# Kernel optimization log

Hardware: AMD Instinct MI355X
Metric: run time of the kernel (lower is better)

Reference implementation:

```python
import jax, jax.numpy as jnp
import numpy as np
import math

L, D, H, HD, F, G, V, P = 15, 512, 64, 8, 2048, 128, 7, 49
B, N = 4, 256


def setup_inputs() -> dict:
    key = jax.random.key(0)
    ks = jax.random.split(key, 24)
    nrm = lambda k, shape, s=0.02: (jax.random.normal(k, shape) * s).astype(jnp.float32)
    inp = {}
    inp["atom_types"] = jax.random.randint(ks[0], (B, N), 0, V)
    inp["coords"] = jax.random.normal(ks[1], (B, N, 3)) * 3.0
    inp["pair_types"] = jax.random.randint(ks[2], (B, N, N), 0, P)
    inp["mask"] = jnp.ones((B, N), dtype=bool)
    # embeddings / pair encoding params
    inp["atom_emb"] = nrm(ks[3], (V, D), 1.0).at[0].set(0.0)  # padding_idx=0
    inp["gaussian_mu"] = jax.random.normal(ks[4], (G,))
    inp["gaussian_sigma"] = jnp.ones((G,)) * 0.1
    inp["pair_a"] = jax.random.normal(ks[5], (P,)) * 0.01
    inp["pair_b"] = jax.random.normal(ks[6], (P,)) * 0.01
    inp["pl_w"] = nrm(ks[7], (G,))
    inp["pl_b"] = jnp.zeros(())
    # stacked per-layer params (leading dim L for lax.scan)
    inp["ln1_g"] = jnp.ones((L, D)); inp["ln1_b"] = jnp.zeros((L, D))
    inp["qkv_w"] = nrm(ks[8], (L, 3 * D, D)); inp["qkv_b"] = jnp.zeros((L, 3 * D))
    inp["pp_w"] = nrm(ks[9], (L, H), 0.1); inp["pp_b"] = jnp.zeros((L, H))
    inp["out_w"] = nrm(ks[10], (L, D, D)); inp["out_b"] = jnp.zeros((L, D))
    inp["ln2_g"] = jnp.ones((L, D)); inp["ln2_b"] = jnp.zeros((L, D))
    inp["ffn_w1"] = nrm(ks[11], (L, F, D)); inp["ffn_b1"] = jnp.zeros((L, F))
    inp["ffn_w2"] = nrm(ks[12], (L, D, F)); inp["ffn_b2"] = jnp.zeros((L, D))
    # SE3 head scalar affines (Linear(1,1) twice) and energy head
    inp["se3_uw"] = jnp.array(0.5); inp["se3_ub"] = jnp.array(0.01)
    inp["se3_ww"] = jnp.array(0.5); inp["se3_wb"] = jnp.array(0.01)
    inp["en_w"] = nrm(ks[13], (D,)); inp["en_b"] = jnp.zeros(())
    return inp


def _layernorm(x, g, b):
    m = x.mean(-1, keepdims=True)
    v = ((x - m) ** 2).mean(-1, keepdims=True)
    return (x - m) / jnp.sqrt(v + 1e-5) * g + b


def reference(atom_types, coords, pair_types, mask,
              atom_emb, gaussian_mu, gaussian_sigma, pair_a, pair_b, pl_w, pl_b,
              ln1_g, ln1_b, qkv_w, qkv_b, pp_w, pp_b, out_w, out_b,
              ln2_g, ln2_b, ffn_w1, ffn_b1, ffn_w2, ffn_b2,
              se3_uw, se3_ub, se3_ww, se3_wb, en_w, en_b):
    b_, n_ = atom_types.shape
    h = atom_emb[atom_types]  # [B,N,D]

    delta = coords[:, :, None, :] - coords[:, None, :, :]  # [B,N,N,3]
    d2 = (delta ** 2).sum(-1)
    dist = jnp.sqrt(jnp.maximum(d2, 1e-12))  # safe norm (grad-safe at 0)
    dist = jnp.where(mask[:, :, None], dist, 0.0)
    da = (pair_a[pair_types] * dist + pair_b[pair_types])[..., None]  # [B,N,N,1]
    gt = jnp.exp(-(da - gaussian_mu) ** 2) / (2.0 * gaussian_sigma ** 2)
    gt = gt / (gaussian_sigma * math.sqrt(2.0 * math.pi))
    gt = gt * mask[:, :, None, None]  # [B,N,N,G]
    pair_repr = gt @ pl_w + pl_b  # [B,N,N]
    pair_mask = mask[:, :, None] & mask[:, None, :]
    pair_repr = pair_repr * pair_mask

    scale = 1.0 / math.sqrt(HD)
    row_mask = mask[:, None, :, None]  # masks query rows, per original code

    def layer(hc, p):
        (l1g, l1b, qw, qb, ppw, ppb, ow, ob, l2g, l2b, w1, b1, w2, b2) = p
        x = _layernorm(hc, l1g, l1b)
        qkv = (x @ qw.T + qb).reshape(b_, n_, 3, H, HD)
        q, k, v = qkv[:, :, 0], qkv[:, :, 1], qkv[:, :, 2]
        scores = jnp.einsum('bnhd,bmhd->bhnm', q, k) * scale
        bias = pair_repr[..., None] * ppw + ppb  # [B,N,N,H]
        scores = scores + bias.transpose(0, 3, 1, 2)
        scores = jnp.where(row_mask, scores, -1e9)
        probs = jax.nn.softmax(scores, axis=-1)
        probs = jnp.where(jnp.isnan(probs), 0.0, probs)
        attn = jnp.einsum('bhnm,bmhd->bnhd', probs, v).reshape(b_, n_, D)
        hc = hc + attn @ ow.T + ob
        x2 = _layernorm(hc, l2g, l2b)
        ffn = jax.nn.gelu(x2 @ w1.T + b1, approximate=False) @ w2.T + b2
        return hc + ffn, None

    h, _ = jax.lax.scan(layer, h, (ln1_g, ln1_b, qkv_w, qkv_b, pp_w, pp_b,
                                   out_w, out_b, ln2_g, ln2_b,
                                   ffn_w1, ffn_b1, ffn_w2, ffn_b2))

    # --- SE3 equivariant head ---
    c = jax.nn.relu(pair_repr)[..., None]  # [B,N,N,1]
    c = c * se3_uw + se3_ub
    c = c * se3_ww + se3_wb
    c = c * mask[:, :, None, None]
    update = (delta * c).sum(axis=2)  # [B,N,3]
    num_valid = mask.sum(-1).astype(coords.dtype)[:, None, None] + 1e-6
    pred_coords = coords + update / num_valid

    cls = h[:, 0, :]
    pred_energy = cls @ en_w + en_b  # [B]
    return pred_coords, pred_energy


if __name__ == '__main__':
    out = reference(**setup_inputs())
    print(out[0].shape, out[1].shape)
```

## Files before the change

### kernel.cpp

```cpp
#include <hip/hip_runtime.h>
#include <hip/hip_bf16.h>
#include <math.h>

#define LAY 15
#define DIM 512
#define NH 64
#define HD 8
#define FF 2048
#define NG 128
#define BATCH 4
#define NTOK 256
#define PSTRIDE 524288

typedef __attribute__((ext_vector_type(8))) short short8;
typedef __attribute__((ext_vector_type(4))) short short4v;
typedef __attribute__((ext_vector_type(2))) short short2v;
typedef __attribute__((ext_vector_type(8))) __bf16 bf16x8;
typedef __attribute__((ext_vector_type(4))) float f32x4;

__device__ inline short f2bs(float f) {
  __bf16 b = (__bf16)f;
  return __builtin_bit_cast(short, b);
}

__global__ __launch_bounds__(256) void embed_kernel(
    const int* __restrict__ types, const float* __restrict__ emb,
    float* __restrict__ h)
{
  int idx = blockIdx.x * 256 + threadIdx.x;
  int token = idx >> 9;
  int d = idx & 511;
  h[idx] = emb[types[token] * DIM + d];
}

__global__ __launch_bounds__(256) void cvt_kernel(
    const float* __restrict__ qkvw, const float* __restrict__ outw,
    const float* __restrict__ w1, const float* __restrict__ w2,
    short* __restrict__ dst)
{
  const int G = 2949120;
  int t0 = blockIdx.x * 256 + threadIdx.x;
  f32x4 f[4];
#pragma unroll
  for (int r = 0; r < 4; ++r) {
    int i = t0 + r * G;
    const float* src; int off;
    if (i < 2949120)      { src = qkvw; off = i; }
    else if (i < 3932160) { src = outw; off = i - 2949120; }
    else if (i < 7864320) { src = w1;   off = i - 3932160; }
    else                  { src = w2;   off = i - 7864320; }
    f[r] = __builtin_nontemporal_load((const f32x4*)src + off);
  }
#pragma unroll
  for (int r = 0; r < 4; ++r) {
    int i = t0 + r * G;
    short4v o;
    o[0] = f2bs(f[r][0]); o[1] = f2bs(f[r][1]);
    o[2] = f2bs(f[r][2]); o[3] = f2bs(f[r][3]);
    *(short4v*)(dst + (size_t)i * 4) = o;
  }
}

__global__ __launch_bounds__(256) void pair_kernel(
    const int* __restrict__ pair_types, const float* __restrict__ coords,
    const float* __restrict__ mu, const float* __restrict__ sigma,
    const float* __restrict__ pa, const float* __restrict__ pb,
    const float* __restrict__ plw, const float* __restrict__ plb,
    const float* __restrict__ uw, const float* __restrict__ ub,
    const float* __restrict__ ww, const float* __restrict__ wb,
    float* __restrict__ pair_repr, float* __restrict__ out)
{
  __shared__ float smu[NG], sw[NG];
  __shared__ float sm[4][3];
  int tid = threadIdx.x;
  if (tid < NG) {
    float sg = sigma[tid];
    smu[tid] = mu[tid];
    sw[tid] = plw[tid] / (2.0f * sg * sg * sg * 2.5066282746310002f);
  }
  __syncthreads();
  int bi = blockIdx.x;
  int b = bi >> 8;
  int j = tid;
  int idx = bi * 256 + j;
  const float* ci = coords + bi * 3;
  const float* cj = coords + (b * NTOK + j) * 3;
  float dx = ci[0] - cj[0], dy = ci[1] - cj[1], dz = ci[2] - cj[2];
  float d2 = dx * dx + dy * dy + dz * dz;
  float dist = sqrtf(fmaxf(d2, 1e-12f));
  int pt = pair_types[idx];
  float da = pa[pt] * dist + pb[pt];
  float acc = 0.0f;
#pragma unroll 8
  for (int g = 0; g < NG; ++g) {
    float t = da - smu[g];
    acc += __expf(-t * t) * sw[g];
  }
  float pr = acc + plb[0];
  pair_repr[idx] = pr;

  float c = fmaxf(pr, 0.0f);
  c = c * uw[0] + ub[0];
  c = c * ww[0] + wb[0];
  float sx = dx * c, sy = dy * c, sz = dz * c;
#pragma unroll
  for (int o = 32; o > 0; o >>= 1) {
    sx += __shfl_xor(sx, o);
    sy += __shfl_xor(sy, o);
    sz += __shfl_xor(sz, o);
  }
  if ((j & 63) == 0) {
    sm[j >> 6][0] = sx; sm[j >> 6][1] = sy; sm[j >> 6][2] = sz;
  }
  __syncthreads();
  if (j < 3) {
    float u = sm[0][j] + sm[1][j] + sm[2][j] + sm[3][j];
    out[bi * 3 + j] = coords[bi * 3 + j] + u * (1.0f / (256.0f + 1e-6f));
  }
}

__global__ __launch_bounds__(256) void pairT_kernel(
    const float* __restrict__ pr, float* __restrict__ prT)
{
  __shared__ float tile[32][33];
  int b = blockIdx.z;
  int i0 = blockIdx.y * 32, j0 = blockIdx.x * 32;
  int tx = threadIdx.x & 31, ty = threadIdx.x >> 5;
#pragma unroll
  for (int r = 0; r < 4; ++r)
    tile[ty + r * 8][tx] = pr[((size_t)(b * NTOK + i0 + ty + r * 8)) * NTOK + j0 + tx];
  __syncthreads();
#pragma unroll
  for (int r = 0; r < 4; ++r)
    prT[((size_t)(b * NTOK + j0 + ty + r * 8)) * NTOK + i0 + tx] = tile[tx][ty + r * 8];
}

__global__ __launch_bounds__(256) void ln_kernel(
    const float* __restrict__ h, const float* __restrict__ g,
    const float* __restrict__ beta, short* __restrict__ x)
{
  int t = blockIdx.x;
  int tid = threadIdx.x;
  float2 v = *(const float2*)&h[(size_t)t * DIM + tid * 2];
  __shared__ float sm[4];
  float s = v.x + v.y;
#pragma unroll
  for (int o = 32; o > 0; o >>= 1) s += __shfl_xor(s, o);
  if ((tid & 63) == 0) sm[tid >> 6] = s;
  __syncthreads();
  float mean = (sm[0] + sm[1] + sm[2] + sm[3]) * (1.0f / 512.0f);
  float d0 = v.x - mean, d1 = v.y - mean;
  float ss = d0 * d0 + d1 * d1;
#pragma unroll
  for (int o = 32; o > 0; o >>= 1) ss += __shfl_xor(ss, o);
  __syncthreads();
  if ((tid & 63) == 0) sm[tid >> 6] = ss;
  __syncthreads();
  float var = (sm[0] + sm[1] + sm[2] + sm[3]) * (1.0f / 512.0f);
  float rstd = rsqrtf(var + 1e-5f);
  float2 gg = *(const float2*)&g[tid * 2];
  float2 bb = *(const float2*)&beta[tid * 2];
  short2v o2;
  o2[0] = f2bs(d0 * rstd * gg.x + bb.x);
  o2[1] = f2bs(d1 * rstd * gg.y + bb.y);
  *(short2v*)&x[(size_t)t * DIM + tid * 2] = o2;
}

__global__ __launch_bounds__(256) void ln_res_kernel(
    float* __restrict__ h, const float* __restrict__ part, int kparts,
    const float* __restrict__ g, const float* __restrict__ beta,
    short* __restrict__ x)
{
  int t = blockIdx.x;
  int tid = threadIdx.x;
  size_t base = (size_t)t * DIM + tid * 2;
  float2 v = *(const float2*)&h[base];
  for (int z = 0; z < kparts; ++z) {
    float2 pz = *(const float2*)&part[(size_t)z * PSTRIDE + base];
    v.x += pz.x; v.y += pz.y;
  }
  *(float2*)&h[base] = v;
  __shared__ float sm[4];
  float s = v.x + v.y;
#pragma unroll
  for (int o = 32; o > 0; o >>= 1) s += __shfl_xor(s, o);
  if ((tid & 63) == 0) sm[tid >> 6] = s;
  __syncthreads();
  float mean = (sm[0] + sm[1] + sm[2] + sm[3]) * (1.0f / 512.0f);
  float d0 = v.x - mean, d1 = v.y - mean;
  float ss = d0 * d0 + d1 * d1;
#pragma unroll
  for (int o = 32; o > 0; o >>= 1) ss += __shfl_xor(ss, o);
  __syncthreads();
  if ((tid & 63) == 0) sm[tid >> 6] = ss;
  __syncthreads();
  float var = (sm[0] + sm[1] + sm[2] + sm[3]) * (1.0f / 512.0f);
  float rstd = rsqrtf(var + 1e-5f);
  float2 gg = *(const float2*)&g[tid * 2];
  float2 bb = *(const float2*)&beta[tid * 2];
  short2v o2;
  o2[0] = f2bs(d0 * rstd * gg.x + bb.x);
  o2[1] = f2bs(d1 * rstd * gg.y + bb.y);
  *(short2v*)&x[base] = o2;
}

template <int MODE, int TSTEPS>
__global__ __launch_bounds__(64) void mm3(
    const short* __restrict__ A, const short* __restrict__ W,
    const float* __restrict__ bias, float* __restrict__ Cf,
    short* __restrict__ Cb, int N, int K)
{
  __shared__ alignas(16) short As[3][2048];
  __shared__ alignas(16) short Bs[3][4096];
  int tid = threadIdx.x;
  int fr = tid & 15, fq = (tid >> 4) & 3;
  int m0 = blockIdx.y * 32, n0 = blockIdx.x * 64;
  int kbeg = blockIdx.z * (TSTEPS * 64);

  auto stage = [&](int p, int k0) {
#pragma unroll
    for (int r = 0; r < 4; ++r) {
      int id = r * 64 + tid;
      int row = id >> 3;
      int col = (id & 7) ^ (row & 7);
      const short* ga = &A[(size_t)(m0 + row) * K + k0 + col * 8];
      __builtin_amdgcn_global_load_lds(
          (const __attribute__((address_space(1))) void*)ga,
          (__attribute__((address_space(3))) void*)&As[p][r * 512],
          16, 0, 0);
    }
#pragma unroll
    for (int r = 0; r < 8; ++r) {
      int id = r * 64 + tid;
      int row = id >> 3;
      int col = (id & 7) ^ (row & 7);
      const short* gw = &W[(size_t)(n0 + row) * K + k0 + col * 8];
      __builtin_amdgcn_global_load_lds(
          (const __attribute__((address_space(1))) void*)gw,
          (__attribute__((address_space(3))) void*)&Bs[p][r * 512],
          16, 0, 0);
    }
  };

  f32x4 acc[2][4];
#pragma unroll
  for (int i = 0; i < 2; ++i)
#pragma unroll
    for (int j = 0; j < 4; ++j) acc[i][j] = (f32x4){0.f, 0.f, 0.f, 0.f};

  int aslot[2][2], bslot[2][4];
#pragma unroll
  for (int s = 0; s < 2; ++s) {
    int c = s * 4 + fq;
#pragma unroll
    for (int i = 0; i < 2; ++i) {
      int m = i * 16 + fr;
      aslot[s][i] = m * 8 + (c ^ (m & 7));
    }
#pragma unroll
    for (int j = 0; j < 4; ++j) {
      int n = j * 16 + fr;
      bslot[s][j] = n * 8 + (c ^ (n & 7));
    }
  }

  stage(0, kbeg);
  stage(1, kbeg + 64);
  stage(2, kbeg + 128);

#pragma unroll
  for (int t = 0; t < TSTEPS; ++t) {
    if (t < TSTEPS - 2)       asm volatile("s_waitcnt vmcnt(24)" ::: "memory");
    else if (t == TSTEPS - 2) asm volatile("s_waitcnt vmcnt(12)" ::: "memory");
    else                      asm volatile("s_waitcnt vmcnt(0)" ::: "memory");
    int p = t % 3;
    short8 af[2][2], bf_[2][4];
#pragma unroll
    for (int s = 0; s < 2; ++s) {
#pragma unroll
      for (int i = 0; i < 2; ++i)
        af[s][i] = *(const short8*)&As[p][aslot[s][i] * 8];
#pragma unroll
      for (int j = 0; j < 4; ++j)
        bf_[s][j] = *(const short8*)&Bs[p][bslot[s][j] * 8];
    }
    asm volatile("s_waitcnt lgkmcnt(0)" ::: "memory");
    __builtin_amdgcn_sched_barrier(0);
    if (t + 3 < TSTEPS) stage(p, kbeg + (t + 3) * 64);
#pragma unroll
    for (int s = 0; s < 2; ++s)
#pragma unroll
      for (int i = 0; i < 2; ++i)
#pragma unroll
        for (int j = 0; j < 4; ++j)
          acc[i][j] = __builtin_amdgcn_mfma_f32_16x16x32_bf16(
              af[s][i], bf_[s][j], acc[i][j], 0, 0, 0);
  }

#pragma unroll
  for (int i = 0; i < 2; ++i) {
#pragma unroll
    for (int j = 0; j < 4; ++j) {
      int col = n0 + j * 16 + fr;
      float bcol = bias[col];
#pragma unroll
      for (int rr = 0; rr < 4; ++rr) {
        int row = m0 + i * 16 + fq * 4 + rr;
        size_t idx = (size_t)row * N + col;
        float v = acc[i][j][rr];
        if (MODE == 2) {
          v += bcol;
          Cb[idx] = f2bs(0.5f * v * (1.0f + erff(v * 0.70710678118654752f)));
        } else if (MODE == 3) {
          Cb[idx] = f2bs(v + bcol);
        } else {
          if (blockIdx.z == 0) v += bcol;
          Cf[(size_t)blockIdx.z * PSTRIDE + idx] = v;
        }
      }
    }
  }
}

__global__ __launch_bounds__(128) void attn_mfma(
    const short* __restrict__ qkv, const float* __restrict__ prT,
    const float* __restrict__ ppw, const float* __restrict__ ppb,
    short* __restrict__ attn)
{
  __shared__ alignas(16) short Kl[256 * 8];
  __shared__ alignas(16) short Ql[128 * 8];
  __shared__ alignas(16) short VT[8 * 264];
  __shared__ alignas(16) short P[2 * 16 * 264];
  __shared__ alignas(16) float linv[32];
  int h = blockIdx.x, b = blockIdx.y;
  int qbase = blockIdx.z * 128;
  int tid = threadIdx.x;

#pragma unroll
  for (int r0 = 0; r0 < 2; ++r0) {
    int r = tid + r0 * 128;
    short8 kv = *(const short8*)&qkv[(size_t)(b * NTOK + r) * 1536 + 512 + h * 8];
    *(short8*)&Kl[r * 8] = kv;
    short8 vv = *(const short8*)&qkv[(size_t)(b * NTOK + r) * 1536 + 1024 + h * 8];
#pragma unroll
    for (int d = 0; d < 8; ++d) VT[d * 264 + r] = vv[d];
  }
  {
    short8 qv = *(const short8*)&qkv[(size_t)(b * NTOK + qbase + tid) * 1536 + h * 8];
    *(short8*)&Ql[tid * 8] = qv;
  }
  __syncthreads();

  int lane = tid & 63, w = tid >> 6;
  int fr = lane & 15, quad = lane >> 4;
  float pw = ppw[h], pbb = ppb[h];
  const float scale = 0.35355339059327373f;
  short8 zero8 = {0, 0, 0, 0, 0, 0, 0, 0};

  short8 vfrag[8];
#pragma unroll
  for (int kc = 0; kc < 8; ++kc)
    vfrag[kc] = (fr < 8) ? *(const short8*)&VT[fr * 264 + kc * 32 + quad * 8]
                         : zero8;

  short* Pw = &P[w * 16 * 264];
  float* lw = &linv[w * 16];

  for (int qt = 0; qt < 4; ++qt) {
    int qloc = w * 64 + qt * 16;
    int qg = qbase + qloc + fr;
    const float* prp = &prT[(size_t)b * 65536 + qg];
    float prv[16][4];
#pragma unroll
    for (int t = 0; t < 16; ++t)
#pragma unroll
      for (int r = 0; r < 4; ++r)
        prv[t][r] = prp[(size_t)(t * 16 + quad * 4 + r) * NTOK];

    short8 qf = zero8;
    if (quad == 0) qf = *(const short8*)&Ql[(qloc + fr) * 8];
    f32x4 sacc[16];
#pragma unroll
    for (int t = 0; t < 16; ++t) {
      short8 kf = zero8;
      if (quad == 0) kf = *(const short8*)&Kl[(t * 16 + fr) * 8];
      sacc[t] = __builtin_amdgcn_mfma_f32_16x16x32_bf16(
          kf, qf, (f32x4){0.f, 0.f, 0.f, 0.f}, 0, 0, 0);
    }

    float l = 0.f;
#pragma unroll
    for (int t = 0; t < 16; ++t) {
      short4v pk;
#pragma unroll
      for (int r = 0; r < 4; ++r) {
        float s = sacc[t][r] * scale + prv[t][r] * pw + pbb;
        float p = __expf(s);
        l += p;
        pk[r] = f2bs(p);
      }
      *(short4v*)&Pw[fr * 264 + t * 16 + quad * 4] = pk;
    }
    l += __shfl_xor(l, 16);
    l += __shfl_xor(l, 32);
    if (lane < 16) lw[fr] = 1.0f / l;

    f32x4 oacc = (f32x4){0.f, 0.f, 0.f, 0.f};
#pragma unroll
    for (int kc = 0; kc < 8; ++kc) {
      short8 pf = *(const short8*)&Pw[fr * 264 + kc * 32 + quad * 8];
      oacc = __builtin_amdgcn_mfma_f32_16x16x32_bf16(pf, vfrag[kc], oacc, 0, 0, 0);
    }
    if (fr < 8) {
      f32x4 li = *(f32x4*)&lw[quad * 4];
#pragma unroll
      for (int r = 0; r < 4; ++r) {
        int q = qbase + qloc + quad * 4 + r;
        attn[(size_t)(b * NTOK + q) * DIM + h * 8 + fr] = f2bs(oacc[r] * li[r]);
      }
    }
  }
}

__global__ __launch_bounds__(256) void energy_kernel(
    const float* __restrict__ h, const float* __restrict__ part,
    const float* __restrict__ enw, const float* __restrict__ enb,
    float* __restrict__ out)
{
  int b = blockIdx.x;
  int tid = threadIdx.x;
  size_t base = (size_t)(b * NTOK) * DIM;
  float x0 = h[base + tid], x1 = h[base + tid + 256];
#pragma unroll
  for (int z = 0; z < 2; ++z) {
    x0 += part[(size_t)z * PSTRIDE + base + tid];
    x1 += part[(size_t)z * PSTRIDE + base + tid + 256];
  }
  float s = x0 * enw[tid] + x1 * enw[tid + 256];
  __shared__ float sm[4];
#pragma unroll
  for (int o = 32; o > 0; o >>= 1) s += __shfl_xor(s, o);
  if ((tid & 63) == 0) sm[tid >> 6] = s;
  __syncthreads();
  if (tid == 0) out[BATCH * NTOK * 3 + b] = sm[0] + sm[1] + sm[2] + sm[3] + enb[0];
}

extern "C" void kernel_launch(void* const* d_in, const int* in_sizes, int n_in,
                              void* d_out, int out_size, void* d_ws, size_t ws_size,
                              hipStream_t stream)
{
  const int*   atom_types = (const int*)d_in[0];
  const float* coords     = (const float*)d_in[1];
  const int*   pair_types = (const int*)d_in[2];
  const float* atom_emb = (const float*)d_in[4];
  const float* gmu  = (const float*)d_in[5];
  const float* gsig = (const float*)d_in[6];
  const float* pa   = (const float*)d_in[7];
  const float* pb   = (const float*)d_in[8];
  const float* plw  = (const float*)d_in[9];
  const float* plb  = (const float*)d_in[10];
  const float* ln1g = (const float*)d_in[11];
  const float* ln1b = (const float*)d_in[12];
  const float* qkvw = (const float*)d_in[13];
  const float* qkvb = (const float*)d_in[14];
  const float* ppw  = (const float*)d_in[15];
  const float* ppb  = (const float*)d_in[16];
  const float* outw = (const float*)d_in[17];
  const float* outb = (const float*)d_in[18];
  const float* ln2g = (const float*)d_in[19];
  const float* ln2b = (const float*)d_in[20];
  const float* w1   = (const float*)d_in[21];
  const float* b1   = (const float*)d_in[22];
  const float* w2   = (const float*)d_in[23];
  const float* b2   = (const float*)d_in[24];
  const float* uw   = (const float*)d_in[25];
  const float* ub   = (const float*)d_in[26];
  const float* sww  = (const float*)d_in[27];
  const float* swb  = (const float*)d_in[28];
  const float* enw  = (const float*)d_in[29];
  const float* enb  = (const float*)d_in[30];

  float* out = (float*)d_out;
  float* ws  = (float*)d_ws;
  float* pair_repr = ws;
  float* prT  = pair_repr + 262144;
  float* h    = prT + 262144;
  float* part = h + 524288;
  short* qkv_bf  = (short*)(part + 4 * 524288);
  short* x_bf    = qkv_bf + 1572864;
  short* attn_bf = x_bf + 524288;
  short* ffn1_bf = attn_bf + 524288;
  short* qkvw_bf = ffn1_bf + 2097152;
  short* outw_bf = qkvw_bf + 11796480;
  short* w1_bf   = outw_bf + 3932160;
  short* w2_bf   = w1_bf + 15728640;

  cvt_kernel<<<11520, 256, 0, stream>>>(qkvw, outw, w1, w2, qkvw_bf);

  embed_kernel<<<2048, 256, 0, stream>>>(atom_types, atom_emb, h);
  pair_kernel<<<1024, 256, 0, stream>>>(pair_types, coords, gmu, gsig, pa, pb,
                                        plw, plb, uw, ub, sww, swb,
                                        pair_repr, out);
  pairT_kernel<<<dim3(8, 8, 4), 256, 0, stream>>>(pair_repr, prT);

  for (int l = 0; l < LAY; ++l) {
    if (l == 0)
      ln_kernel<<<1024, 256, 0, stream>>>(h, ln1g, ln1b, x_bf);
    else
      ln_res_kernel<<<1024, 256, 0, stream>>>(h, part, 2,
                                              ln1g + l * DIM, ln1b + l * DIM, x_bf);
    mm3<3, 8><<<dim3(24, 32, 1), 64, 0, stream>>>(
        x_bf, qkvw_bf + (size_t)l * 1536 * DIM, qkvb + l * 1536, nullptr, qkv_bf,
        1536, DIM);
    attn_mfma<<<dim3(NH, BATCH, 2), 128, 0, stream>>>(
        qkv_bf, prT, ppw + l * NH, ppb + l * NH, attn_bf);
    mm3<4, 4><<<dim3(8, 32, 2), 64, 0, stream>>>(
        attn_bf, outw_bf + (size_t)l * DIM * DIM, outb + l * DIM, part, nullptr,
        DIM, DIM);
    ln_res_kernel<<<1024, 256, 0, stream>>>(h, part, 2,
                                            ln2g + l * DIM, ln2b + l * DIM, x_bf);
    mm3<2, 8><<<dim3(32, 32, 1), 64, 0, stream>>>(
        x_bf, w1_bf + (size_t)l * FF * DIM, b1 + l * FF, nullptr, ffn1_bf,
        FF, DIM);
    mm3<4, 16><<<dim3(8, 32, 2), 64, 0, stream>>>(
        ffn1_bf, w2_bf + (size_t)l * DIM * FF, b2 + l * DIM, part, nullptr,
        DIM, FF);
  }
  energy_kernel<<<BATCH, 256, 0, stream>>>(h, part, enw, enb, out);
}
```

Before: 1.113 ms.

## Load GEMM fragments directly from global into registers, dropping LDS staging

The mm3 GEMM kernel no longer stages A and W tiles through a triple-buffered LDS ring with global_load_lds. Each lane now loads its MFMA operand fragments straight from global memory into registers, double-buffered across k-steps. This removes LDS traffic, the explicit waitcnt choreography and the LDS footprint, which could raise occupancy. In exchange, global loads are less coalesced (16-byte strided row reads) and the compiler's own waits replace the manual pipelining.

```diff
diff --git a/kernel.cpp b/kernel.cpp
--- a/kernel.cpp
+++ b/kernel.cpp
@@ -210,83 +210,32 @@
     const float* __restrict__ bias, float* __restrict__ Cf,
     short* __restrict__ Cb, int N, int K)
 {
-  __shared__ alignas(16) short As[3][2048];
-  __shared__ alignas(16) short Bs[3][4096];
-  int tid = threadIdx.x;
-  int fr = tid & 15, fq = (tid >> 4) & 3;
+  int tid = threadIdx.x;
+  int fr = tid & 15, fq = tid >> 4;
   int m0 = blockIdx.y * 32, n0 = blockIdx.x * 64;
   int kbeg = blockIdx.z * (TSTEPS * 64);
 
-  auto stage = [&](int p, int k0) {
-#pragma unroll
-    for (int r = 0; r < 4; ++r) {
-      int id = r * 64 + tid;
-      int row = id >> 3;
-      int col = (id & 7) ^ (row & 7);
-      const short* ga = &A[(size_t)(m0 + row) * K + k0 + col * 8];
-      __builtin_amdgcn_global_load_lds(
-          (const __attribute__((address_space(1))) void*)ga,
-          (__attribute__((address_space(3))) void*)&As[p][r * 512],
-          16, 0, 0);
-    }
-#pragma unroll
-    for (int r = 0; r < 8; ++r) {
-      int id = r * 64 + tid;
-      int row = id >> 3;
-      int col = (id & 7) ^ (row & 7);
-      const short* gw = &W[(size_t)(n0 + row) * K + k0 + col * 8];
-      __builtin_amdgcn_global_load_lds(
-          (const __attribute__((address_space(1))) void*)gw,
-          (__attribute__((address_space(3))) void*)&Bs[p][r * 512],
-          16, 0, 0);
+  const short* Ab = A + (size_t)(m0 + fr) * K + fq * 8 + kbeg;
+  const short* Wb = W + (size_t)(n0 + fr) * K + fq * 8 + kbeg;
+
+  f32x4 acc[2][4];
+#pragma unroll
+  for (int i = 0; i < 2; ++i)
+#pragma unroll
+    for (int j = 0; j < 4; ++j) acc[i][j] = (f32x4){0.f, 0.f, 0.f, 0.f};
+
+  auto LD = [&](short8 (&af)[2][2], short8 (&bf)[2][4], int k0) {
+#pragma unroll
+    for (int s = 0; s < 2; ++s) {
+#pragma unroll
+      for (int i = 0; i < 2; ++i)
+        af[s][i] = *(const short8*)(Ab + (size_t)i * 16 * K + k0 + s * 32);
+#pragma unroll
+      for (int j = 0; j < 4; ++j)
+        bf[s][j] = *(const short8*)(Wb + (size_t)j * 16 * K + k0 + s * 32);
     }
   };
-
-  f32x4 acc[2][4];
-#pragma unroll
-  for (int i = 0; i < 2; ++i)
-#pragma unroll
-    for (int j = 0; j < 4; ++j) acc[i][j] = (f32x4){0.f, 0.f, 0.f, 0.f};
-
-  int aslot[2][2], bslot[2][4];
-#pragma unroll
-  for (int s = 0; s < 2; ++s) {
-    int c = s * 4 + fq;
-#pragma unroll
-    for (int i = 0; i < 2; ++i) {
-      int m = i * 16 + fr;
-      aslot[s][i] = m * 8 + (c ^ (m & 7));
-    }
-#pragma unroll
-    for (int j = 0; j < 4; ++j) {
-      int n = j * 16 + fr;
-      bslot[s][j] = n * 8 + (c ^ (n & 7));
-    }
-  }
-
-  stage(0, kbeg);
-  stage(1, kbeg + 64);
-  stage(2, kbeg + 128);
-
-#pragma unroll
-  for (int t = 0; t < TSTEPS; ++t) {
-    if (t < TSTEPS - 2)       asm volatile("s_waitcnt vmcnt(24)" ::: "memory");
-    else if (t == TSTEPS - 2) asm volatile("s_waitcnt vmcnt(12)" ::: "memory");
-    else                      asm volatile("s_waitcnt vmcnt(0)" ::: "memory");
-    int p = t % 3;
-    short8 af[2][2], bf_[2][4];
-#pragma unroll
-    for (int s = 0; s < 2; ++s) {
-#pragma unroll
-      for (int i = 0; i < 2; ++i)
-        af[s][i] = *(const short8*)&As[p][aslot[s][i] * 8];
-#pragma unroll
-      for (int j = 0; j < 4; ++j)
-        bf_[s][j] = *(const short8*)&Bs[p][bslot[s][j] * 8];
-    }
-    asm volatile("s_waitcnt lgkmcnt(0)" ::: "memory");
-    __builtin_amdgcn_sched_barrier(0);
-    if (t + 3 < TSTEPS) stage(p, kbeg + (t + 3) * 64);
+  auto FM = [&](short8 (&af)[2][2], short8 (&bf)[2][4]) {
 #pragma unroll
     for (int s = 0; s < 2; ++s)
 #pragma unroll
@@ -294,7 +243,20 @@
 #pragma unroll
         for (int j = 0; j < 4; ++j)
           acc[i][j] = __builtin_amdgcn_mfma_f32_16x16x32_bf16(
-              af[s][i], bf_[s][j], acc[i][j], 0, 0, 0);
+              af[s][i], bf[s][j], acc[i][j], 0, 0, 0);
+  };
+
+  short8 aA[2][2], bA[2][4], aB[2][2], bB[2][4];
+  LD(aA, bA, 0);
+#pragma unroll
+  for (int t = 0; t < TSTEPS; ++t) {
+    if ((t & 1) == 0) {
+      if (t + 1 < TSTEPS) LD(aB, bB, (t + 1) * 64);
+      FM(aA, bA);
+    } else {
+      if (t + 1 < TSTEPS) LD(aA, bA, (t + 1) * 64);
+      FM(aB, bB);
+    }
   }
 
 #pragma unroll
```

New measurement: 1.413 ms. 1.27x slower.

## Fuse residual-add and LayerNorm into the QKV and FFN1 GEMM prologue

Applied to the files above, without the earlier changes.

Replaces the separate ln/ln_res kernels with a fused GEMM (mm3ln) that loads the full 32-row activation slab, adds the split-K partials, computes LayerNorm in registers and writes bf16 straight into shared memory before the MFMA loop. The residual stream ping-pongs between two buffers (hA/hB), and only the blockIdx.x==0 column of blocks writes it back. This drops two kernel launches per layer and the x_bf round trip through global memory. In exchange, every column block recomputes the LayerNorm for its rows, which adds redundant reads of h and the partials. The single-pass variance formula is also less numerically robust.

```diff
diff --git a/kernel.cpp b/kernel.cpp
--- a/kernel.cpp
+++ b/kernel.cpp
@@ -135,73 +135,156 @@
     prT[((size_t)(b * NTOK + j0 + ty + r * 8)) * NTOK + i0 + tx] = tile[tx][ty + r * 8];
 }
 
-__global__ __launch_bounds__(256) void ln_kernel(
-    const float* __restrict__ h, const float* __restrict__ g,
-    const float* __restrict__ beta, short* __restrict__ x)
-{
-  int t = blockIdx.x;
+template <int MODE, int NP>
+__global__ __launch_bounds__(64) void mm3ln(
+    const float* __restrict__ hsrc, const float* __restrict__ parts,
+    float* __restrict__ hout,
+    const float* __restrict__ lng, const float* __restrict__ lnb,
+    const short* __restrict__ W, const float* __restrict__ bias,
+    short* __restrict__ Cb, int N)
+{
+  constexpr int TS = 8;
+  __shared__ alignas(16) short Af[32 * 512];
+  __shared__ alignas(16) short Bs[2][4096];
   int tid = threadIdx.x;
-  float2 v = *(const float2*)&h[(size_t)t * DIM + tid * 2];
-  __shared__ float sm[4];
-  float s = v.x + v.y;
-#pragma unroll
-  for (int o = 32; o > 0; o >>= 1) s += __shfl_xor(s, o);
-  if ((tid & 63) == 0) sm[tid >> 6] = s;
-  __syncthreads();
-  float mean = (sm[0] + sm[1] + sm[2] + sm[3]) * (1.0f / 512.0f);
-  float d0 = v.x - mean, d1 = v.y - mean;
-  float ss = d0 * d0 + d1 * d1;
-#pragma unroll
-  for (int o = 32; o > 0; o >>= 1) ss += __shfl_xor(ss, o);
-  __syncthreads();
-  if ((tid & 63) == 0) sm[tid >> 6] = ss;
-  __syncthreads();
-  float var = (sm[0] + sm[1] + sm[2] + sm[3]) * (1.0f / 512.0f);
-  float rstd = rsqrtf(var + 1e-5f);
-  float2 gg = *(const float2*)&g[tid * 2];
-  float2 bb = *(const float2*)&beta[tid * 2];
-  short2v o2;
-  o2[0] = f2bs(d0 * rstd * gg.x + bb.x);
-  o2[1] = f2bs(d1 * rstd * gg.y + bb.y);
-  *(short2v*)&x[(size_t)t * DIM + tid * 2] = o2;
-}
-
-__global__ __launch_bounds__(256) void ln_res_kernel(
-    float* __restrict__ h, const float* __restrict__ part, int kparts,
-    const float* __restrict__ g, const float* __restrict__ beta,
-    short* __restrict__ x)
-{
-  int t = blockIdx.x;
-  int tid = threadIdx.x;
-  size_t base = (size_t)t * DIM + tid * 2;
-  float2 v = *(const float2*)&h[base];
-  for (int z = 0; z < kparts; ++z) {
-    float2 pz = *(const float2*)&part[(size_t)z * PSTRIDE + base];
-    v.x += pz.x; v.y += pz.y;
-  }
-  *(float2*)&h[base] = v;
-  __shared__ float sm[4];
-  float s = v.x + v.y;
-#pragma unroll
-  for (int o = 32; o > 0; o >>= 1) s += __shfl_xor(s, o);
-  if ((tid & 63) == 0) sm[tid >> 6] = s;
-  __syncthreads();
-  float mean = (sm[0] + sm[1] + sm[2] + sm[3]) * (1.0f / 512.0f);
-  float d0 = v.x - mean, d1 = v.y - mean;
-  float ss = d0 * d0 + d1 * d1;
-#pragma unroll
-  for (int o = 32; o > 0; o >>= 1) ss += __shfl_xor(ss, o);
-  __syncthreads();
-  if ((tid & 63) == 0) sm[tid >> 6] = ss;
-  __syncthreads();
-  float var = (sm[0] + sm[1] + sm[2] + sm[3]) * (1.0f / 512.0f);
-  float rstd = rsqrtf(var + 1e-5f);
-  float2 gg = *(const float2*)&g[tid * 2];
-  float2 bb = *(const float2*)&beta[tid * 2];
-  short2v o2;
-  o2[0] = f2bs(d0 * rstd * gg.x + bb.x);
-  o2[1] = f2bs(d1 * rstd * gg.y + bb.y);
-  *(short2v*)&x[base] = o2;
+  int fr = tid & 15, fq = (tid >> 4) & 3;
+  int m0 = blockIdx.y * 32, n0 = blockIdx.x * 64;
+
+  auto stageB = [&](int p, int k0) {
+#pragma unroll
+    for (int r = 0; r < 8; ++r) {
+      int id = r * 64 + tid;
+      int row = id >> 3;
+      int col = (id & 7) ^ (row & 7);
+      const short* gw = &W[(size_t)(n0 + row) * 512 + k0 + col * 8];
+      __builtin_amdgcn_global_load_lds(
+          (const __attribute__((address_space(1))) void*)gw,
+          (__attribute__((address_space(3))) void*)&Bs[p][r * 512],
+          16, 0, 0);
+    }
+  };
+  stageB(0, 0);
+  stageB(1, 64);
+
+  {
+    const float* hb  = hsrc + (size_t)m0 * DIM + tid * 8;
+    const float* pb0 = parts + (size_t)m0 * DIM + tid * 8;
+    float* ho = (hout != nullptr && blockIdx.x == 0)
+                    ? hout + (size_t)m0 * DIM + tid * 8 : nullptr;
+    f32x4 g0 = *(const f32x4*)(lng + tid * 8);
+    f32x4 g1 = *(const f32x4*)(lng + tid * 8 + 4);
+    f32x4 b0 = *(const f32x4*)(lnb + tid * 8);
+    f32x4 b1 = *(const f32x4*)(lnb + tid * 8 + 4);
+#pragma unroll 2
+    for (int r = 0; r < 32; ++r) {
+      f32x4 v0 = *(const f32x4*)(hb + r * DIM);
+      f32x4 v1 = *(const f32x4*)(hb + r * DIM + 4);
+      if (NP == 2) {
+        v0 += *(const f32x4*)(pb0 + r * DIM) +
+              *(const f32x4*)(pb0 + PSTRIDE + r * DIM);
+        v1 += *(const f32x4*)(pb0 + r * DIM + 4) +
+              *(const f32x4*)(pb0 + PSTRIDE + r * DIM + 4);
+      }
+      if (ho) {
+        *(f32x4*)(ho + r * DIM) = v0;
+        *(f32x4*)(ho + r * DIM + 4) = v1;
+      }
+      float s  = ((v0[0] + v0[1]) + (v0[2] + v0[3])) +
+                 ((v1[0] + v1[1]) + (v1[2] + v1[3]));
+      float ss = (v0[0]*v0[0] + v0[1]*v0[1] + v0[2]*v0[2] + v0[3]*v0[3]) +
+                 (v1[0]*v1[0] + v1[1]*v1[1] + v1[2]*v1[2] + v1[3]*v1[3]);
+#pragma unroll
+      for (int o = 32; o > 0; o >>= 1) {
+        s  += __shfl_xor(s, o);
+        ss += __shfl_xor(ss, o);
+      }
+      float mean = s * (1.0f / 512.0f);
+      float var  = ss * (1.0f / 512.0f) - mean * mean;
+      float rstd = rsqrtf(fmaxf(var, 0.0f) + 1e-5f);
+      short8 o8;
+      o8[0] = f2bs((v0[0] - mean) * rstd * g0[0] + b0[0]);
+      o8[1] = f2bs((v0[1] - mean) * rstd * g0[1] + b0[1]);
+      o8[2] = f2bs((v0[2] - mean) * rstd * g0[2] + b0[2]);
+      o8[3] = f2bs((v0[3] - mean) * rstd * g0[3] + b0[3]);
+      o8[4] = f2bs((v1[0] - mean) * rstd * g1[0] + b1[0]);
+      o8[5] = f2bs((v1[1] - mean) * rstd * g1[1] + b1[1]);
+      o8[6] = f2bs((v1[2] - mean) * rstd * g1[2] + b1[2]);
+      o8[7] = f2bs((v1[3] - mean) * rstd * g1[3] + b1[3]);
+      int slot = r * 64 + (tid ^ (r & 7));
+      *(short8*)&Af[slot * 8] = o8;
+    }
+  }
+  asm volatile("s_waitcnt lgkmcnt(0)" ::: "memory");
+  __builtin_amdgcn_sched_barrier(0);
+
+  f32x4 acc[2][4];
+#pragma unroll
+  for (int i = 0; i < 2; ++i)
+#pragma unroll
+    for (int j = 0; j < 4; ++j) acc[i][j] = (f32x4){0.f, 0.f, 0.f, 0.f};
+
+  int abase[2][2], bslot[2][4];
+#pragma unroll
+  for (int s = 0; s < 2; ++s) {
+    int c = s * 4 + fq;
+#pragma unroll
+    for (int i = 0; i < 2; ++i) {
+      int mf = i * 16 + fr;
+      abase[s][i] = mf * 64 + (c ^ (mf & 7));
+    }
+#pragma unroll
+    for (int j = 0; j < 4; ++j) {
+      int n = j * 16 + fr;
+      bslot[s][j] = n * 8 + (c ^ (n & 7));
+    }
+  }
+
+#pragma unroll
+  for (int t = 0; t < TS; ++t) {
+    if (t == TS - 1) asm volatile("s_waitcnt vmcnt(0)" ::: "memory");
+    else             asm volatile("s_waitcnt vmcnt(8)" ::: "memory");
+    int p = t & 1;
+    short8 af[2][2], bf_[2][4];
+#pragma unroll
+    for (int s = 0; s < 2; ++s) {
+#pragma unroll
+      for (int i = 0; i < 2; ++i)
+        af[s][i] = *(const short8*)&Af[(abase[s][i] + t * 8) * 8];
+#pragma unroll
+      for (int j = 0; j < 4; ++j)
+        bf_[s][j] = *(const short8*)&Bs[p][bslot[s][j] * 8];
+    }
+    asm volatile("s_waitcnt lgkmcnt(0)" ::: "memory");
+    __builtin_amdgcn_sched_barrier(0);
+    if (t + 2 < TS) stageB(p, (t + 2) * 64);
+#pragma unroll
+    for (int s = 0; s < 2; ++s)
+#pragma unroll
+      for (int i = 0; i < 2; ++i)
+#pragma unroll
+        for (int j = 0; j < 4; ++j)
+          acc[i][j] = __builtin_amdgcn_mfma_f32_16x16x32_bf16(
+              af[s][i], bf_[s][j], acc[i][j], 0, 0, 0);
+  }
+
+#pragma unroll
+  for (int i = 0; i < 2; ++i) {
+#pragma unroll
+    for (int j = 0; j < 4; ++j) {
+      int col = n0 + j * 16 + fr;
+      float bcol = bias[col];
+#pragma unroll
+      for (int rr = 0; rr < 4; ++rr) {
+        int row = m0 + i * 16 + fq * 4 + rr;
+        size_t idx = (size_t)row * N + col;
+        float v = acc[i][j][rr] + bcol;
+        if (MODE == 2)
+          Cb[idx] = f2bs(0.5f * v * (1.0f + erff(v * 0.70710678118654752f)));
+        else
+          Cb[idx] = f2bs(v);
+      }
+    }
+  }
 }
 
 template <int MODE, int TSTEPS>
@@ -484,8 +567,9 @@
   float* ws  = (float*)d_ws;
   float* pair_repr = ws;
   float* prT  = pair_repr + 262144;
-  float* h    = prT + 262144;
-  float* part = h + 524288;
+  float* hA   = prT + 262144;
+  float* part = hA + 524288;
+  float* hB   = part + 2 * 524288;
   short* qkv_bf  = (short*)(part + 4 * 524288);
   short* x_bf    = qkv_bf + 1572864;
   short* attn_bf = x_bf + 524288;
@@ -497,7 +581,7 @@
 
   cvt_kernel<<<11520, 256, 0, stream>>>(qkvw, outw, w1, w2, qkvw_bf);
 
-  embed_kernel<<<2048, 256, 0, stream>>>(atom_types, atom_emb, h);
+  embed_kernel<<<2048, 256, 0, stream>>>(atom_types, atom_emb, hA);
   pair_kernel<<<1024, 256, 0, stream>>>(pair_types, coords, gmu, gsig, pa, pb,
                                         plw, plb, uw, ub, sww, swb,
                                         pair_repr, out);
@@ -505,26 +589,24 @@
 
   for (int l = 0; l < LAY; ++l) {
     if (l == 0)
-      ln_kernel<<<1024, 256, 0, stream>>>(h, ln1g, ln1b, x_bf);
+      mm3ln<3, 0><<<dim3(24, 32), 64, 0, stream>>>(
+          hA, part, hB, ln1g, ln1b,
+          qkvw_bf, qkvb, qkv_bf, 1536);
     else
-      ln_res_kernel<<<1024, 256, 0, stream>>>(h, part, 2,
-                                              ln1g + l * DIM, ln1b + l * DIM, x_bf);
-    mm3<3, 8><<<dim3(24, 32, 1), 64, 0, stream>>>(
-        x_bf, qkvw_bf + (size_t)l * 1536 * DIM, qkvb + l * 1536, nullptr, qkv_bf,
-        1536, DIM);
+      mm3ln<3, 2><<<dim3(24, 32), 64, 0, stream>>>(
+          hA, part, hB, ln1g + l * DIM, ln1b + l * DIM,
+          qkvw_bf + (size_t)l * 1536 * DIM, qkvb + l * 1536, qkv_bf, 1536);
     attn_mfma<<<dim3(NH, BATCH, 2), 128, 0, stream>>>(
         qkv_bf, prT, ppw + l * NH, ppb + l * NH, attn_bf);
     mm3<4, 4><<<dim3(8, 32, 2), 64, 0, stream>>>(
         attn_bf, outw_bf + (size_t)l * DIM * DIM, outb + l * DIM, part, nullptr,
         DIM, DIM);
-    ln_res_kernel<<<1024, 256, 0, stream>>>(h, part, 2,
-                                            ln2g + l * DIM, ln2b + l * DIM, x_bf);
-    mm3<2, 8><<<dim3(32, 32, 1), 64, 0, stream>>>(
-        x_bf, w1_bf + (size_t)l * FF * DIM, b1 + l * FF, nullptr, ffn1_bf,
-        FF, DIM);
+    mm3ln<2, 2><<<dim3(32, 32), 64, 0, stream>>>(
+        hB, part, hA, ln2g + l * DIM, ln2b + l * DIM,
+        w1_bf + (size_t)l * FF * DIM, b1 + l * FF, ffn1_bf, FF);
     mm3<4, 16><<<dim3(8, 32, 2), 64, 0, stream>>>(
         ffn1_bf, w2_bf + (size_t)l * DIM * FF, b2 + l * DIM, part, nullptr,
         DIM, FF);
   }
-  energy_kernel<<<BATCH, 256, 0, stream>>>(h, part, enw, enb, out);
-}
+  energy_kernel<<<BATCH, 256, 0, stream>>>(hA, part, enw, enb, out);
+}
```

Measured after the change: 1.879 ms. 1.69x slower.
